# Kernel optimization log

Measured on AMD Instinct MI355X. Metric: run time of the kernel, lower is better.

The kernel has to match this reference:

```python
import jax, jax.numpy as jnp
import numpy as np

EPS = 1e-6
N_HEAD, N_KV_HEAD = 16, 4
VE_GATE_CH = 12

def rmsnorm(x):
    return x * jax.lax.rsqrt(jnp.mean(x * x, axis=-1, keepdims=True) + EPS)

def apply_rotary_emb(x, cos, sin):
    half = x.shape[-1] // 2
    x1, x2 = x[..., :half], x[..., half:]
    return jnp.concatenate([x1 * cos + x2 * sin, -x1 * sin + x2 * cos], axis=-1)

def setup_inputs():
    key = jax.random.key(0)
    ks = jax.random.split(key, 8)
    B, S, D = 2, 2048, 1024
    H, KVH = N_HEAD, N_KV_HEAD
    hd = D // H
    x = jax.random.normal(ks[0], (B, S, D), jnp.float32)
    ve = jax.random.normal(ks[1], (B, S, KVH * hd), jnp.float32)
    # real rotary tables, broadcastable over [B,S,H,hd//2]
    inv_freq = 1.0 / (10000.0 ** (np.arange(hd // 2, dtype=np.float32) / (hd // 2)))
    ang = np.arange(S, dtype=np.float32)[:, None] * inv_freq[None, :]  # [S, hd//2]
    cos = jnp.asarray(np.cos(ang))[:, None, :]  # [S,1,hd//2]
    sin = jnp.asarray(np.sin(ang))[:, None, :]
    std = 0.02
    Wq = jax.random.normal(ks[2], (D, H * hd), jnp.float32) * std
    Wk = jax.random.normal(ks[3], (D, KVH * hd), jnp.float32) * std
    Wv = jax.random.normal(ks[4], (D, KVH * hd), jnp.float32) * std
    Wo = jax.random.normal(ks[5], (D, D), jnp.float32) * std
    Wg = jax.random.normal(ks[6], (VE_GATE_CH, KVH), jnp.float32) * std
    return {"x": x, "ve": ve, "cos": cos, "sin": sin, "Wq": Wq, "Wk": Wk,
            "Wv": Wv, "Wo": Wo, "Wg": Wg, "window_size": 512}

def reference(x, ve, cos, sin, Wq, Wk, Wv, Wo, Wg, window_size):
    B, S, D = x.shape
    H, KVH = N_HEAD, N_KV_HEAD
    hd = D // H
    q = (x @ Wq).reshape(B, S, H, hd)
    k = (x @ Wk).reshape(B, S, KVH, hd)
    v = (x @ Wv).reshape(B, S, KVH, hd)
    # value-embedding gating
    gate = 3.0 * jax.nn.sigmoid(x[..., :VE_GATE_CH] @ Wg)  # [B,S,KVH]
    v = v + gate[..., None] * ve.reshape(B, S, KVH, hd)
    # RoPE + QK rmsnorm * 1.2
    q = rmsnorm(apply_rotary_emb(q, cos, sin)) * 1.2
    k = rmsnorm(apply_rotary_emb(k, cos, sin)) * 1.2
    # GQA head repeat (repeat_interleave over head dim)
    rep = H // KVH
    k = jnp.repeat(k, rep, axis=2)  # [B,S,H,hd]
    v = jnp.repeat(v, rep, axis=2)
    scale = 1.0 / np.sqrt(hd).astype(np.float32)
    scores = jnp.einsum('bqhd,bkhd->bhqk', q, k) * scale  # [B,H,S,S]
    pos = jnp.arange(S)
    allow = (pos[None, :] <= pos[:, None]) & (pos[None, :] >= pos[:, None] - window_size + 1)
    scores = jnp.where(allow[None, None], scores, -jnp.inf)
    attn = jax.nn.softmax(scores, axis=-1)
    y = jnp.einsum('bhqk,bkhd->bqhd', attn, v).reshape(B, S, D)
    return y @ Wo
```

## Files before the change

### kernel.cpp

```cpp
#include <hip/hip_runtime.h>
#include <hip/hip_bf16.h>
#include <cstddef>
#include <cstdint>


typedef short v8s __attribute__((ext_vector_type(8)));
typedef float v4f __attribute__((ext_vector_type(4)));

__device__ __forceinline__ ushort f2b(float f) {
  __hip_bfloat16 h = __float2bfloat16(f);
  return reinterpret_cast<ushort&>(h);
}

__device__ __forceinline__ void async16(const ushort* g, ushort* l) {
  __builtin_amdgcn_global_load_lds(
      (__attribute__((address_space(1))) void*)(uintptr_t)(const void*)g,
      (__attribute__((address_space(3))) void*)(uintptr_t)(void*)l, 16, 0, 0);
}

__global__ __launch_bounds__(256) void cvt_gate(
    const float* __restrict__ x, ushort* __restrict__ xb,
    const float* __restrict__ Wg, float* __restrict__ gates)
{
  const int bs = blockIdx.x, t = threadIdx.x;
  const float* row = x + (size_t)bs * 1024;
  float4 v = *(const float4*)(row + t * 4);
  ushort4 o;
  o.x = f2b(v.x); o.y = f2b(v.y); o.z = f2b(v.z); o.w = f2b(v.w);
  *(ushort4*)(xb + (size_t)bs * 1024 + t * 4) = o;
  if (t < 4) {
    float g = 0.f;
#pragma unroll
    for (int i = 0; i < 12; ++i) g += row[i] * Wg[i * 4 + t];
    gates[bs * 4 + t] = 3.0f / (1.0f + __expf(-g));
  }
}

__global__ __launch_bounds__(256) void prep_cs(
    const float* __restrict__ cosp, const float* __restrict__ sinp,
    float2* __restrict__ cs)
{
  const int i = blockIdx.x * 256 + threadIdx.x;
  cs[i] = make_float2(cosp[i], sinp[i]);
}

__global__ __launch_bounds__(256) void transpose_cvt4(
    const float* __restrict__ Wq, const float* __restrict__ Wk,
    const float* __restrict__ Wv, const float* __restrict__ Wo,
    ushort* __restrict__ Wqt, ushort* __restrict__ Wkt,
    ushort* __restrict__ Wvt, ushort* __restrict__ Wot)
{
  __shared__ ushort tile[32][33];
  const int z = blockIdx.z;
  const float* W = (z == 0) ? Wq : (z == 1) ? Wo : (z == 2) ? Wk : Wv;
  ushort* Wt     = (z == 0) ? Wqt : (z == 1) ? Wot : (z == 2) ? Wkt : Wvt;
  const int N = (z < 2) ? 1024 : 256;
  const int n0 = blockIdx.x * 32, k0 = blockIdx.y * 32;
  if (n0 >= N) return;
  const int tx = threadIdx.x & 31, ty = threadIdx.x >> 5;
#pragma unroll
  for (int i = 0; i < 4; ++i) {
    const int k = ty + i * 8;
    tile[k][tx] = f2b(W[(size_t)(k0 + k) * N + n0 + tx]);
  }
  __syncthreads();
#pragma unroll
  for (int i = 0; i < 4; ++i) {
    const int n = ty + i * 8;
    Wt[(size_t)(n0 + n) * 1024 + k0 + tx] = tile[tx][n];
  }
}

__device__ __forceinline__ void gemm_mainloop(
    const ushort* __restrict__ A, const ushort* __restrict__ Bt,
    int K, int m0, int n0, ushort (*As)[64], ushort (*Bs)[64],
    v4f acc[4][4])
{
  const int t = threadIdx.x;
  const int lane = t & 63, wave = t >> 6;
  const int wr = wave >> 1, wc = wave & 1;
  const int quad = lane >> 4, l16 = lane & 15;
  const int l8 = lane >> 3, c8 = (lane & 7) * 8;

  const ushort* ap[4];
  const ushort* bp[4];
  ushort* al[4];
  ushort* bl[4];
#pragma unroll
  for (int i = 0; i < 4; ++i) {
    const int row = (wave * 4 + i) * 8 + l8;
    ap[i] = A  + (size_t)(m0 + row) * K + c8;
    bp[i] = Bt + (size_t)(n0 + row) * K + c8;
    al[i] = &As[(wave * 4 + i) * 8][0];
    bl[i] = &Bs[(wave * 4 + i) * 8][0];
  }

  for (int k0 = 0; k0 < K; k0 += 64) {
#pragma unroll
    for (int i = 0; i < 4; ++i) {
      async16(ap[i] + k0, al[i]);
      async16(bp[i] + k0, bl[i]);
    }
    __syncthreads();
#pragma unroll
    for (int ks = 0; ks < 2; ++ks) {
      v8s af[4], bf[4];
#pragma unroll
      for (int i = 0; i < 4; ++i) {
        af[i] = *(const v8s*)&As[wr * 64 + i * 16 + l16][ks * 32 + quad * 8];
        bf[i] = *(const v8s*)&Bs[wc * 64 + i * 16 + l16][ks * 32 + quad * 8];
      }
#pragma unroll
      for (int mt = 0; mt < 4; ++mt)
#pragma unroll
        for (int nt = 0; nt < 4; ++nt)
          acc[mt][nt] = __builtin_amdgcn_mfma_f32_16x16x32_bf16(
              af[mt], bf[nt], acc[mt][nt], 0, 0, 0);
    }
    __syncthreads();
  }
}

__global__ __launch_bounds__(256) void gemm_qkv_fused(
    const ushort* __restrict__ A, const ushort* __restrict__ Bt,
    const float2* __restrict__ cs, const float* __restrict__ gates,
    const float* __restrict__ ve,
    ushort* __restrict__ qb, ushort* __restrict__ kb, ushort* __restrict__ vb)
{
  __shared__ ushort As[128][64];
  __shared__ ushort Bs[128][64];
  const int m0 = blockIdx.x * 128, n0 = blockIdx.y * 128;
  const int lane = threadIdx.x & 63, wave = threadIdx.x >> 6;
  const int wr = wave >> 1, wc = wave & 1;
  const int quad = lane >> 4, l16 = lane & 15;

  v4f acc[4][4];
#pragma unroll
  for (int i = 0; i < 4; ++i)
#pragma unroll
    for (int j = 0; j < 4; ++j) acc[i][j] = (v4f){0.f, 0.f, 0.f, 0.f};

  gemm_mainloop(A, Bt, 1024, m0, n0, As, Bs, acc);

  const int sec = blockIdx.y;
  const int head_col = n0 + wc * 64;

  if (sec < 10) {
    const bool isQ = (sec < 8);
    const int h = (head_col - (isQ ? 0 : 1024)) >> 6;
    ushort* dst = isQ ? qb : kb;
    const int ld = isQ ? 1024 : 256;
#pragma unroll
    for (int mt = 0; mt < 4; ++mt)
#pragma unroll
      for (int r = 0; r < 4; ++r) {
        const int row = m0 + wr * 64 + mt * 16 + quad * 4 + r;
        const int s = row & 2047;
        const float2 cs0 = cs[s * 32 + l16];
        const float2 cs1 = cs[s * 32 + 16 + l16];
        const float x10 = acc[mt][0][r], x11 = acc[mt][1][r];
        const float x20 = acc[mt][2][r], x21 = acc[mt][3][r];
        float ss = x10 * x10 + x11 * x11 + x20 * x20 + x21 * x21;
        ss += __shfl_xor(ss, 1);
        ss += __shfl_xor(ss, 2);
        ss += __shfl_xor(ss, 4);
        ss += __shfl_xor(ss, 8);
        const float rs = rsqrtf(ss * (1.0f / 64.0f) + 1e-6f) * 1.2f;
        ushort* dp = dst + (size_t)row * ld + h * 64 + l16;
        dp[0]  = f2b((x10 * cs0.x + x20 * cs0.y) * rs);
        dp[16] = f2b((x11 * cs1.x + x21 * cs1.y) * rs);
        dp[32] = f2b((-x10 * cs0.y + x20 * cs0.x) * rs);
        dp[48] = f2b((-x11 * cs1.y + x21 * cs1.x) * rs);
      }
  } else {
    const int kvh = (head_col - 1280) >> 6;
#pragma unroll
    for (int mt = 0; mt < 4; ++mt)
#pragma unroll
      for (int r = 0; r < 4; ++r) {
        const int row = m0 + wr * 64 + mt * 16 + quad * 4 + r;
        const float gate = gates[row * 4 + kvh];
        const float* vep = ve + (size_t)row * 256 + kvh * 64 + l16;
        ushort* dp = vb + (size_t)row * 256 + kvh * 64 + l16;
#pragma unroll
        for (int nt = 0; nt < 4; ++nt)
          dp[nt * 16] = f2b(acc[mt][nt][r] + gate * vep[nt * 16]);
      }
  }
}

__global__ __launch_bounds__(256) void gemm_wo(
    const ushort* __restrict__ A, const ushort* __restrict__ Bt,
    float* __restrict__ C)
{
  __shared__ ushort As[128][64];
  __shared__ ushort Bs[128][64];
  const int m0 = blockIdx.x * 128, n0 = blockIdx.y * 128;
  const int lane = threadIdx.x & 63, wave = threadIdx.x >> 6;
  const int wr = wave >> 1, wc = wave & 1;
  const int quad = lane >> 4, l16 = lane & 15;

  v4f acc[4][4];
#pragma unroll
  for (int i = 0; i < 4; ++i)
#pragma unroll
    for (int j = 0; j < 4; ++j) acc[i][j] = (v4f){0.f, 0.f, 0.f, 0.f};

  gemm_mainloop(A, Bt, 1024, m0, n0, As, Bs, acc);

#pragma unroll
  for (int mt = 0; mt < 4; ++mt)
#pragma unroll
    for (int r = 0; r < 4; ++r) {
      float* cp = C + (size_t)(m0 + wr * 64 + mt * 16 + quad * 4 + r) * 1024
                    + n0 + wc * 64 + l16;
#pragma unroll
      for (int nt = 0; nt < 4; ++nt) cp[nt * 16] = acc[mt][nt][r];
    }
}

__global__ __launch_bounds__(256) void transpose_v(
    const ushort* __restrict__ vb, ushort* __restrict__ vtb)
{
  __shared__ ushort L[64][72];
  const int s0 = blockIdx.x * 64, kvh = blockIdx.y, b = blockIdx.z;
  const int t = threadIdx.x;
#pragma unroll
  for (int i = 0; i < 2; ++i) {
    const int cc = t + i * 256;
    const int srow = cc >> 3, c8 = (cc & 7) * 8;
    *(int4*)&L[srow][c8] =
        *(const int4*)(vb + ((size_t)(b * 2048 + s0 + srow)) * 256 + kvh * 64 + c8);
  }
  __syncthreads();
#pragma unroll
  for (int i = 0; i < 2; ++i) {
    const int cc = t + i * 256;
    const int drow = cc >> 3, s8 = (cc & 7) * 8;
    ushort w[8];
#pragma unroll
    for (int jj = 0; jj < 8; ++jj) w[jj] = L[s8 + jj][drow];
    *(int4*)(vtb + ((size_t)((b * 4 + kvh) * 64 + drow)) * 2048 + s0 + s8) =
        *(int4*)w;
  }
}

__global__ __launch_bounds__(256) void attn_mfma(
    const ushort* __restrict__ qb, const ushort* __restrict__ kb,
    const ushort* __restrict__ vtb, ushort* __restrict__ yb,
    const int* __restrict__ wptr)
{
  __shared__ ushort Ks[64][72];
  __shared__ ushort Vt[80][72];
  __shared__ ushort Ps[128][72];
  const int qt = blockIdx.x, h = blockIdx.y, b = blockIdx.z;
  const int kvh = h >> 2, q0 = qt * 128;
  const int t = threadIdx.x, lane = t & 63, wave = t >> 6;
  const int quad = lane >> 4, l16 = lane & 15;
  const int Wwin = *wptr;

  v8s qf[2][2];
#pragma unroll
  for (int s = 0; s < 2; ++s) {
    const ushort* qp = qb + ((size_t)(b * 2048 + q0 + wave * 32 + s * 16 + l16)) * 1024
                          + h * 64 + quad * 8;
    qf[s][0] = *(const v8s*)qp;
    qf[s][1] = *(const v8s*)(qp + 32);
  }

  if (t < 128) {
    const int row = 64 + (t >> 3), c8 = (t & 7) * 8;
    const int v = (row == 64) ? 0x3F803F80 : 0;
    int4 w; w.x = v; w.y = v; w.z = v; w.w = v;
    *(int4*)&Vt[row][c8] = w;
  }

  v4f o[2][5];
#pragma unroll
  for (int s = 0; s < 2; ++s)
#pragma unroll
    for (int d = 0; d < 5; ++d) o[s][d] = (v4f){0.f, 0.f, 0.f, 0.f};

  const int lo = q0 - Wwin + 1;
  const int kt0 = (lo > 0) ? (lo >> 6) : 0;
  const int kt1 = (q0 + 127) >> 6;

  for (int kt = kt0; kt <= kt1; ++kt) {
#pragma unroll
    for (int i = 0; i < 2; ++i) {
      const int cc = t + i * 256;
      const int r8 = cc >> 3, c8 = (cc & 7) * 8;
      *(int4*)&Ks[r8][c8] =
          *(const int4*)(kb + ((size_t)(b * 2048 + kt * 64 + r8)) * 256 + kvh * 64 + c8);
      *(int4*)&Vt[r8][c8] =
          *(const int4*)(vtb + ((size_t)((b * 4 + kvh) * 64 + r8)) * 2048 + kt * 64 + c8);
    }
    __syncthreads();

    const bool needs_mask = (kt * 64 + 63 > q0) || (kt * 64 < q0 + 128 - Wwin);

#pragma unroll
    for (int s = 0; s < 2; ++s) {
      const int qrow = q0 + wave * 32 + s * 16 + l16;
      ushort* prow = &Ps[wave * 32 + s * 16 + l16][0];
#pragma unroll
      for (int nt = 0; nt < 4; ++nt) {
        v8s kf0 = *(const v8s*)&Ks[nt * 16 + l16][quad * 8];
        v8s kf1 = *(const v8s*)&Ks[nt * 16 + l16][32 + quad * 8];
        v4f st = (v4f){0.f, 0.f, 0.f, 0.f};
        st = __builtin_amdgcn_mfma_f32_16x16x32_bf16(kf0, qf[s][0], st, 0, 0, 0);
        st = __builtin_amdgcn_mfma_f32_16x16x32_bf16(kf1, qf[s][1], st, 0, 0, 0);
        float p[4];
#pragma unroll
        for (int r = 0; r < 4; ++r) {
          p[r] = __expf(fmaf(st[r], 0.125f, -12.0f));
          if (needs_mask) {
            const int k = kt * 64 + nt * 16 + quad * 4 + r;
            const bool ok = (k <= qrow) && (k > qrow - Wwin);
            p[r] = ok ? p[r] : 0.0f;
          }
        }
        uint2 w;
        w.x = (uint)f2b(p[0]) | ((uint)f2b(p[1]) << 16);
        w.y = (uint)f2b(p[2]) | ((uint)f2b(p[3]) << 16);
        *(uint2*)(prow + nt * 16 + quad * 4) = w;
      }
    }

    v8s pf[2][2];
#pragma unroll
    for (int s = 0; s < 2; ++s) {
      pf[s][0] = *(const v8s*)&Ps[wave * 32 + s * 16 + l16][quad * 8];
      pf[s][1] = *(const v8s*)&Ps[wave * 32 + s * 16 + l16][32 + quad * 8];
    }
#pragma unroll
    for (int dt = 0; dt < 5; ++dt) {
      v8s vf0 = *(const v8s*)&Vt[dt * 16 + l16][quad * 8];
      v8s vf1 = *(const v8s*)&Vt[dt * 16 + l16][32 + quad * 8];
#pragma unroll
      for (int s = 0; s < 2; ++s) {
        o[s][dt] = __builtin_amdgcn_mfma_f32_16x16x32_bf16(pf[s][0], vf0, o[s][dt], 0, 0, 0);
        o[s][dt] = __builtin_amdgcn_mfma_f32_16x16x32_bf16(pf[s][1], vf1, o[s][dt], 0, 0, 0);
      }
    }
    __syncthreads();
  }

#pragma unroll
  for (int s = 0; s < 2; ++s)
#pragma unroll
    for (int r = 0; r < 4; ++r) {
      const float l = __shfl(o[s][4][r], lane & 48);
      const float inv = 1.0f / l;
      ushort* yp = yb + ((size_t)(b * 2048 + q0 + wave * 32 + s * 16 + quad * 4 + r)) * 1024
                      + h * 64 + l16;
#pragma unroll
      for (int dt = 0; dt < 4; ++dt) yp[dt * 16] = f2b(o[s][dt][r] * inv);
    }
}

extern "C" void kernel_launch(void* const* d_in, const int* in_sizes, int n_in,
                              void* d_out, int out_size, void* d_ws, size_t ws_size,
                              hipStream_t stream)
{
  const float* x    = (const float*)d_in[0];
  const float* ve   = (const float*)d_in[1];
  const float* cosp = (const float*)d_in[2];
  const float* sinp = (const float*)d_in[3];
  const float* Wq   = (const float*)d_in[4];
  const float* Wk   = (const float*)d_in[5];
  const float* Wv   = (const float*)d_in[6];
  const float* Wo   = (const float*)d_in[7];
  const float* Wg   = (const float*)d_in[8];
  const int*   win  = (const int*)d_in[9];
  float* out = (float*)d_out;

  char* p = (char*)d_ws;
  ushort* xb    = (ushort*)p;  p += (size_t)4194304 * 2;
  ushort* qb    = (ushort*)p;  p += (size_t)4194304 * 2;
  ushort* yb    = (ushort*)p;  p += (size_t)4194304 * 2;
  ushort* kb    = (ushort*)p;  p += (size_t)1048576 * 2;
  ushort* vb    = (ushort*)p;  p += (size_t)1048576 * 2;
  ushort* vtb   = (ushort*)p;  p += (size_t)1048576 * 2;
  ushort* Wqkvt = (ushort*)p;  p += (size_t)1536 * 1024 * 2;
  ushort* Wot   = (ushort*)p;  p += (size_t)1048576 * 2;
  float2* cs    = (float2*)p;  p += (size_t)65536 * 8;
  float*  gates = (float*)p;

  cvt_gate<<<4096, 256, 0, stream>>>(x, xb, Wg, gates);
  prep_cs<<<256, 256, 0, stream>>>(cosp, sinp, cs);
  transpose_cvt4<<<dim3(32, 32, 4), 256, 0, stream>>>(
      Wq, Wk, Wv, Wo,
      Wqkvt, Wqkvt + (size_t)1024 * 1024, Wqkvt + (size_t)1280 * 1024, Wot);

  gemm_qkv_fused<<<dim3(32, 12), 256, 0, stream>>>(xb, Wqkvt, cs, gates, ve,
                                                   qb, kb, vb);
  transpose_v<<<dim3(32, 4, 2), 256, 0, stream>>>(vb, vtb);

  attn_mfma<<<dim3(16, 16, 2), 256, 0, stream>>>(qb, kb, vtb, yb, win);

  gemm_wo<<<dim3(32, 8), 256, 0, stream>>>(yb, Wot, out);
}
```

Before: 177.5 us.

## Merge prep kernels into one launch, use bit-trick bf16 rounding and exp2

```diff
diff --git a/kernel.cpp b/kernel.cpp
--- a/kernel.cpp
+++ b/kernel.cpp
@@ -7,9 +7,15 @@
 typedef short v8s __attribute__((ext_vector_type(8)));
 typedef float v4f __attribute__((ext_vector_type(4)));
 
-__device__ __forceinline__ ushort f2b(float f) {
-  __hip_bfloat16 h = __float2bfloat16(f);
-  return reinterpret_cast<ushort&>(h);
+__device__ __forceinline__ ushort b1(float a) {
+  uint u = __float_as_uint(a);
+  return (ushort)((u + 0x7FFFu + ((u >> 16) & 1u)) >> 16);
+}
+__device__ __forceinline__ uint bpack(float lo, float hi) {
+  uint ul = __float_as_uint(lo), uh = __float_as_uint(hi);
+  ul = (ul + 0x7FFFu + ((ul >> 16) & 1u)) >> 16;
+  uh = (uh + 0x7FFFu + ((uh >> 16) & 1u)) & 0xFFFF0000u;
+  return ul | uh;
 }
 
 __device__ __forceinline__ void async16(const ushort* g, ushort* l) {
@@ -18,50 +24,49 @@
       (__attribute__((address_space(3))) void*)(uintptr_t)(void*)l, 16, 0, 0);
 }
 
-__global__ __launch_bounds__(256) void cvt_gate(
+__global__ __launch_bounds__(256) void prep_all(
     const float* __restrict__ x, ushort* __restrict__ xb,
-    const float* __restrict__ Wg, float* __restrict__ gates)
-{
-  const int bs = blockIdx.x, t = threadIdx.x;
-  const float* row = x + (size_t)bs * 1024;
-  float4 v = *(const float4*)(row + t * 4);
-  ushort4 o;
-  o.x = f2b(v.x); o.y = f2b(v.y); o.z = f2b(v.z); o.w = f2b(v.w);
-  *(ushort4*)(xb + (size_t)bs * 1024 + t * 4) = o;
-  if (t < 4) {
-    float g = 0.f;
-#pragma unroll
-    for (int i = 0; i < 12; ++i) g += row[i] * Wg[i * 4 + t];
-    gates[bs * 4 + t] = 3.0f / (1.0f + __expf(-g));
-  }
-}
-
-__global__ __launch_bounds__(256) void prep_cs(
+    const float* __restrict__ Wg, float* __restrict__ gates,
     const float* __restrict__ cosp, const float* __restrict__ sinp,
-    float2* __restrict__ cs)
-{
-  const int i = blockIdx.x * 256 + threadIdx.x;
-  cs[i] = make_float2(cosp[i], sinp[i]);
-}
-
-__global__ __launch_bounds__(256) void transpose_cvt4(
+    float2* __restrict__ cs,
     const float* __restrict__ Wq, const float* __restrict__ Wk,
     const float* __restrict__ Wv, const float* __restrict__ Wo,
     ushort* __restrict__ Wqt, ushort* __restrict__ Wkt,
     ushort* __restrict__ Wvt, ushort* __restrict__ Wot)
 {
+  const int bx = blockIdx.x, t = threadIdx.x;
+  if (bx < 4096) {
+    const float* row = x + (size_t)bx * 1024;
+    float4 v = *(const float4*)(row + t * 4);
+    ushort4 o;
+    o.x = b1(v.x); o.y = b1(v.y); o.z = b1(v.z); o.w = b1(v.w);
+    *(ushort4*)(xb + (size_t)bx * 1024 + t * 4) = o;
+    if (t < 4) {
+      float g = 0.f;
+#pragma unroll
+      for (int i = 0; i < 12; ++i) g += row[i] * Wg[i * 4 + t];
+      gates[bx * 4 + t] = 3.0f / (1.0f + __expf(-g));
+    }
+    return;
+  }
+  if (bx < 4352) {
+    const int i = (bx - 4096) * 256 + t;
+    cs[i] = make_float2(cosp[i], sinp[i]);
+    return;
+  }
   __shared__ ushort tile[32][33];
-  const int z = blockIdx.z;
-  const float* W = (z == 0) ? Wq : (z == 1) ? Wo : (z == 2) ? Wk : Wv;
-  ushort* Wt     = (z == 0) ? Wqt : (z == 1) ? Wot : (z == 2) ? Wkt : Wvt;
-  const int N = (z < 2) ? 1024 : 256;
-  const int n0 = blockIdx.x * 32, k0 = blockIdx.y * 32;
-  if (n0 >= N) return;
-  const int tx = threadIdx.x & 31, ty = threadIdx.x >> 5;
+  int u = bx - 4352;
+  const float* W; ushort* Wt; int N, xx, yy;
+  if (u < 1024)      { W = Wq; Wt = Wqt; N = 1024; xx = u & 31; yy = u >> 5; }
+  else if (u < 2048) { u -= 1024; W = Wo; Wt = Wot; N = 1024; xx = u & 31; yy = u >> 5; }
+  else if (u < 2304) { u -= 2048; W = Wk; Wt = Wkt; N = 256;  xx = u & 7;  yy = u >> 3; }
+  else               { u -= 2304; W = Wv; Wt = Wvt; N = 256;  xx = u & 7;  yy = u >> 3; }
+  const int n0 = xx * 32, k0 = yy * 32;
+  const int tx = t & 31, ty = t >> 5;
 #pragma unroll
   for (int i = 0; i < 4; ++i) {
     const int k = ty + i * 8;
-    tile[k][tx] = f2b(W[(size_t)(k0 + k) * N + n0 + tx]);
+    tile[k][tx] = b1(W[(size_t)(k0 + k) * N + n0 + tx]);
   }
   __syncthreads();
 #pragma unroll
@@ -167,10 +172,10 @@
         ss += __shfl_xor(ss, 8);
         const float rs = rsqrtf(ss * (1.0f / 64.0f) + 1e-6f) * 1.2f;
         ushort* dp = dst + (size_t)row * ld + h * 64 + l16;
-        dp[0]  = f2b((x10 * cs0.x + x20 * cs0.y) * rs);
-        dp[16] = f2b((x11 * cs1.x + x21 * cs1.y) * rs);
-        dp[32] = f2b((-x10 * cs0.y + x20 * cs0.x) * rs);
-        dp[48] = f2b((-x11 * cs1.y + x21 * cs1.x) * rs);
+        dp[0]  = b1((x10 * cs0.x + x20 * cs0.y) * rs);
+        dp[16] = b1((x11 * cs1.x + x21 * cs1.y) * rs);
+        dp[32] = b1((-x10 * cs0.y + x20 * cs0.x) * rs);
+        dp[48] = b1((-x11 * cs1.y + x21 * cs1.x) * rs);
       }
   } else {
     const int kvh = (head_col - 1280) >> 6;
@@ -184,7 +189,7 @@
         ushort* dp = vb + (size_t)row * 256 + kvh * 64 + l16;
 #pragma unroll
         for (int nt = 0; nt < 4; ++nt)
-          dp[nt * 16] = f2b(acc[mt][nt][r] + gate * vep[nt * 16]);
+          dp[nt * 16] = b1(acc[mt][nt][r] + gate * vep[nt * 16]);
       }
   }
 }
@@ -313,7 +318,7 @@
         float p[4];
 #pragma unroll
         for (int r = 0; r < 4; ++r) {
-          p[r] = __expf(fmaf(st[r], 0.125f, -12.0f));
+          p[r] = exp2f(fmaf(st[r], 0.18033688011f, -17.31234049107f));
           if (needs_mask) {
             const int k = kt * 64 + nt * 16 + quad * 4 + r;
             const bool ok = (k <= qrow) && (k > qrow - Wwin);
@@ -321,8 +326,8 @@
           }
         }
         uint2 w;
-        w.x = (uint)f2b(p[0]) | ((uint)f2b(p[1]) << 16);
-        w.y = (uint)f2b(p[2]) | ((uint)f2b(p[3]) << 16);
+        w.x = bpack(p[0], p[1]);
+        w.y = bpack(p[2], p[3]);
         *(uint2*)(prow + nt * 16 + quad * 4) = w;
       }
     }
@@ -355,7 +360,7 @@
       ushort* yp = yb + ((size_t)(b * 2048 + q0 + wave * 32 + s * 16 + quad * 4 + r)) * 1024
                       + h * 64 + l16;
 #pragma unroll
-      for (int dt = 0; dt < 4; ++dt) yp[dt * 16] = f2b(o[s][dt][r] * inv);
+      for (int dt = 0; dt < 4; ++dt) yp[dt * 16] = b1(o[s][dt][r] * inv);
     }
 }
 
@@ -387,10 +392,8 @@
   float2* cs    = (float2*)p;  p += (size_t)65536 * 8;
   float*  gates = (float*)p;
 
-  cvt_gate<<<4096, 256, 0, stream>>>(x, xb, Wg, gates);
-  prep_cs<<<256, 256, 0, stream>>>(cosp, sinp, cs);
-  transpose_cvt4<<<dim3(32, 32, 4), 256, 0, stream>>>(
-      Wq, Wk, Wv, Wo,
+  prep_all<<<6912, 256, 0, stream>>>(
+      x, xb, Wg, gates, cosp, sinp, cs, Wq, Wk, Wv, Wo,
       Wqkvt, Wqkvt + (size_t)1024 * 1024, Wqkvt + (size_t)1280 * 1024, Wot);
 
   gemm_qkv_fused<<<dim3(32, 12), 256, 0, stream>>>(xb, Wqkvt, cs, gates, ve,
```

Result: no change. 174.5 us (-1.7%).
